# Kernel tuning notes

Hardware: AMD Instinct MI355X
Metric: run time of the kernel (lower is better)

The kernel has to match this reference:

```python
import jax, jax.numpy as jnp
import numpy as np

BATCH, SEQ = 4, 2048
D_MODEL, D_STATE, D_CONV, HEADDIM = 512, 128, 4, 64
D_INNER = 1024          # expand * d_model
NHEADS = 16             # d_inner / headdim
CONV_DIM = D_INNER + 2 * D_STATE   # 1280 (ngroups=1)
D_IN_PROJ = 2 * D_INNER + 2 * D_STATE + NHEADS  # 2320


def setup_inputs() -> dict:
    key = jax.random.key(0)
    ks = jax.random.split(key, 7)
    x = jax.random.normal(ks[0], (BATCH, SEQ, D_MODEL), jnp.float32)
    norm_weight = jnp.ones((D_MODEL,), jnp.float32)
    in_proj_w = jax.random.normal(ks[1], (D_IN_PROJ, D_MODEL), jnp.float32) * 0.02
    conv_w = jax.random.normal(ks[2], (CONV_DIM, 1, D_CONV), jnp.float32) * 0.2
    conv_b = jnp.zeros((CONV_DIM,), jnp.float32)
    dt_bias = jax.random.normal(ks[3], (NHEADS,), jnp.float32) * 0.1
    A_log = jnp.log(jax.random.uniform(ks[4], (NHEADS,), jnp.float32, 1.0, 16.0))
    D_param = jnp.ones((NHEADS,), jnp.float32)
    gated_norm_weight = jnp.ones((D_INNER,), jnp.float32)
    out_proj_w = jax.random.normal(ks[5], (D_MODEL, D_INNER), jnp.float32) * 0.02
    return dict(x=x, norm_weight=norm_weight, in_proj_w=in_proj_w, conv_w=conv_w,
                conv_b=conv_b, dt_bias=dt_bias, A_log=A_log, D_param=D_param,
                gated_norm_weight=gated_norm_weight, out_proj_w=out_proj_w)


def _rmsnorm(x, w, eps):
    return w * (x * jax.lax.rsqrt(jnp.mean(x * x, axis=-1, keepdims=True) + eps))


def _mamba2_forward(x, norm_weight, in_proj_w, conv_w, conv_b, dt_bias,
                    A_log, D_param, gated_norm_weight, out_proj_w):
    b, l, _ = x.shape
    u = _rmsnorm(x, norm_weight, 1e-6)                       # pre-norm (eps=1e-6)
    zxbcdt = u @ in_proj_w.T                                 # (b,l,2320)
    z = zxbcdt[..., :D_INNER]                                # gate
    xBC = zxbcdt[..., D_INNER:D_INNER + CONV_DIM]            # (b,l,1280)
    dt = zxbcdt[..., D_INNER + CONV_DIM:]                    # (b,l,nheads)
    dt = jax.nn.softplus(dt + dt_bias)

    # causal depthwise conv1d over time + SiLU
    conv = jax.lax.conv_general_dilated(
        xBC.transpose(0, 2, 1), conv_w, window_strides=(1,),
        padding=[(D_CONV - 1, 0)], feature_group_count=CONV_DIM,
        dimension_numbers=('NCH', 'OIH', 'NCH'))
    xBC = jax.nn.silu((conv + conv_b[None, :, None]).transpose(0, 2, 1))

    xs = xBC[..., :D_INNER].reshape(b, l, NHEADS, HEADDIM)   # (b,l,h,p)
    Bmat = xBC[..., D_INNER:D_INNER + D_STATE]               # (b,l,n)
    Cmat = xBC[..., D_INNER + D_STATE:]                      # (b,l,n)

    A = -jnp.exp(A_log)                                      # (h,)
    dA = jnp.exp(dt * A)                                     # (b,l,h)
    dtx = dt[..., None] * xs                                 # (b,l,h,p)

    def step(h, inp):
        dA_t, dtx_t, B_t, C_t = inp                          # (b,h),(b,h,p),(b,n),(b,n)
        h = h * dA_t[..., None, None] + dtx_t[..., None] * B_t[:, None, None, :]
        y = jnp.einsum('bhpn,bn->bhp', h, C_t)
        return h, y

    h0 = jnp.zeros((b, NHEADS, HEADDIM, D_STATE), x.dtype)
    _, ys = jax.lax.scan(step, h0, (dA.transpose(1, 0, 2), dtx.transpose(1, 0, 2, 3),
                                    Bmat.transpose(1, 0, 2), Cmat.transpose(1, 0, 2)))
    y = ys.transpose(1, 0, 2, 3) + xs * D_param[None, None, :, None]  # D skip
    y = y.reshape(b, l, D_INNER)

    y = _rmsnorm(y * jax.nn.silu(z), gated_norm_weight, 1e-5)  # RMSNormGated (eps=1e-5)
    return x + y @ out_proj_w.T                                # residual


def reference(x, norm_weight, in_proj_w, conv_w, conv_b, dt_bias,
              A_log, D_param, gated_norm_weight, out_proj_w):
    return _mamba2_forward(x, norm_weight, in_proj_w, conv_w, conv_b, dt_bias,
                           A_log, D_param, gated_norm_weight, out_proj_w)
```

## Files before the change

### kernel.cpp

```cpp
#include <hip/hip_runtime.h>
#include <cstdint>
#include <cstddef>

#define B_ 4
#define L_ 2048
#define DMODEL 512
#define DINNER 1024
#define DSTATE 128
#define NH 16
#define HD 64
#define CONVDIM 1280
#define NPROJ 2320
#define NPAD 2432
#define ML (B_*L_)
#define Q_ 64
#define NCH 32

typedef __bf16 bf16x8 __attribute__((ext_vector_type(8)));
typedef float f32x4 __attribute__((ext_vector_type(4)));

__device__ __forceinline__ float bf2f(ushort u) {
  union { unsigned int i; float f; } v; v.i = ((unsigned int)u) << 16; return v.f;
}
__device__ __forceinline__ ushort f2bf(float f) {
  union { float f; unsigned int i; } v; v.f = f;
  unsigned int u = v.i;
  unsigned int r = (u + 0x7fffu + ((u >> 16) & 1u)) >> 16;
  return (ushort)r;
}
__device__ __forceinline__ float siluf(float x) { return x / (1.f + __expf(-x)); }

__device__ __forceinline__ void gl_lds16(const void* g, void* l) {
  __builtin_amdgcn_global_load_lds(
      (const __attribute__((address_space(1))) unsigned int*)g,
      (__attribute__((address_space(3))) unsigned int*)l,
      16, 0, 0);
}

__global__ __launch_bounds__(256) void k_cvt(const float* __restrict__ wi, const float* __restrict__ wo,
                                             ushort* __restrict__ oi, ushort* __restrict__ oo) {
  int idx = blockIdx.x * 256 + threadIdx.x;
  const int n1 = NPAD * DMODEL;
  if (idx < n1) {
    int n = idx / DMODEL, k = idx % DMODEL;
    oi[idx] = f2bf((n < NPROJ) ? wi[(size_t)n * DMODEL + k] : 0.f);
  } else {
    int j = idx - n1;
    if (j < DMODEL * DINNER) oo[j] = f2bf(wo[j]);
  }
}

__global__ __launch_bounds__(256) void k_rmsnorm(const float* __restrict__ x, const float* __restrict__ w,
                                                 ushort* __restrict__ u) {
  int row = blockIdx.x * 4 + (threadIdx.x >> 6);
  int lane = threadIdx.x & 63;
  const float* xr = x + (size_t)row * DMODEL + lane * 8;
  float4 a = *(const float4*)xr;
  float4 b = *(const float4*)(xr + 4);
  float ss = a.x*a.x + a.y*a.y + a.z*a.z + a.w*a.w + b.x*b.x + b.y*b.y + b.z*b.z + b.w*b.w;
  ss += __shfl_xor(ss, 1);  ss += __shfl_xor(ss, 2);  ss += __shfl_xor(ss, 4);
  ss += __shfl_xor(ss, 8);  ss += __shfl_xor(ss, 16); ss += __shfl_xor(ss, 32);
  float sc = rsqrtf(ss * (1.f / DMODEL) + 1e-6f);
  const float* wr = w + lane * 8;
  float4 wa = *(const float4*)wr;
  float4 wb = *(const float4*)(wr + 4);
  union { ushort s[8]; int4 v; } o;
  o.s[0] = f2bf(a.x * wa.x * sc); o.s[1] = f2bf(a.y * wa.y * sc);
  o.s[2] = f2bf(a.z * wa.z * sc); o.s[3] = f2bf(a.w * wa.w * sc);
  o.s[4] = f2bf(b.x * wb.x * sc); o.s[5] = f2bf(b.y * wb.y * sc);
  o.s[6] = f2bf(b.z * wb.z * sc); o.s[7] = f2bf(b.w * wb.w * sc);
  *(int4*)(u + (size_t)row * DMODEL + lane * 8) = o.v;
}

template <int EPI, int BM, int BN, int MR, int NR>
__global__ __launch_bounds__(256) void gemm_bt(const ushort* __restrict__ A, const ushort* __restrict__ Bm,
                                               void* __restrict__ Cout, const float* __restrict__ resid,
                                               int M, int N, int K, int gx) {
  constexpr int WM = MR * 16, WN = NR * 16;
  constexpr int WAVES_N = BN / WN;
  constexpr int CH_A = BM / 8, CH_B = BN / 8;
  constexpr int PER_A = CH_A / 4, PER_B = CH_B / 4;
  constexpr int SL = PER_A + PER_B;
  __shared__ __align__(16) ushort lA[2][BM * 64];
  __shared__ __align__(16) ushort lB[2][BN * 64];
  const int nwg = gridDim.x;
  const int cpx = nwg >> 3;
  const int bid = blockIdx.x;
  const int swz = (bid & 7) * cpx + (bid >> 3);
  const int n0 = (swz % gx) * BN, m0 = (swz / gx) * BM;
  const int t = threadIdx.x;
  const int wave = t >> 6, lane = t & 63;
  const int wr = wave / WAVES_N, wc = wave % WAVES_N;
  const int r3 = lane >> 3;
  const int ce = (((lane & 7) ^ r3) << 3);
  const int nt = K >> 6;
  f32x4 acc[MR][NR] = {};
  auto stage = [&](int buf, int k0) {
#pragma unroll
    for (int i = 0; i < PER_A; ++i) {
      int chunk = wave * PER_A + i;
      int row = chunk * 8 + r3;
      gl_lds16(A + (size_t)(m0 + row) * K + k0 + ce, (char*)&lA[buf][0] + chunk * 1024);
    }
#pragma unroll
    for (int i = 0; i < PER_B; ++i) {
      int chunk = wave * PER_B + i;
      int row = chunk * 8 + r3;
      gl_lds16(Bm + (size_t)(n0 + row) * K + k0 + ce, (char*)&lB[buf][0] + chunk * 1024);
    }
  };
  stage(0, 0);
  const int rsel = lane & 15;
  const int kswz = (lane & 7) << 3;
  for (int kt = 0; kt < nt; ++kt) {
    const int cur = kt & 1;
    if (kt + 1 < nt) {
      stage(cur ^ 1, (kt + 1) << 6);
      if constexpr (SL == 8) asm volatile("s_waitcnt vmcnt(8)" ::: "memory");
      else if constexpr (SL == 6) asm volatile("s_waitcnt vmcnt(6)" ::: "memory");
      else asm volatile("s_waitcnt vmcnt(0)" ::: "memory");
    } else {
      asm volatile("s_waitcnt vmcnt(0)" ::: "memory");
    }
    __builtin_amdgcn_s_barrier();
#pragma unroll
    for (int kk = 0; kk < 64; kk += 32) {
      const int ksel = kk + ((lane >> 4) << 3);
      const int kcol = ksel ^ kswz;
      bf16x8 af[MR], bfr[NR];
#pragma unroll
      for (int m = 0; m < MR; ++m)
        af[m] = *reinterpret_cast<const bf16x8*>(&lA[cur][(wr * WM + m * 16 + rsel) * 64 + kcol]);
#pragma unroll
      for (int n = 0; n < NR; ++n)
        bfr[n] = *reinterpret_cast<const bf16x8*>(&lB[cur][(wc * WN + n * 16 + rsel) * 64 + kcol]);
#pragma unroll
      for (int m = 0; m < MR; ++m)
#pragma unroll
        for (int n = 0; n < NR; ++n)
          acc[m][n] = __builtin_amdgcn_mfma_f32_16x16x32_bf16(af[m], bfr[n], acc[m][n], 0, 0, 0);
    }
    __builtin_amdgcn_s_barrier();
  }
  const int rowf = (lane >> 4) * 4;
  const int coln = lane & 15;
#pragma unroll
  for (int m = 0; m < MR; ++m) {
#pragma unroll
    for (int n = 0; n < NR; ++n) {
      int gm_base = m0 + wr * WM + m * 16 + rowf;
      int gn = n0 + wc * WN + n * 16 + coln;
#pragma unroll
      for (int r = 0; r < 4; ++r) {
        int gm = gm_base + r;
        float v = acc[m][n][r];
        if (EPI == 0) {
          ((ushort*)Cout)[(size_t)gm * N + gn] = f2bf(v);
        } else {
          ((float*)Cout)[(size_t)gm * N + gn] = v + resid[(size_t)gm * N + gn];
        }
      }
    }
  }
}

__global__ __launch_bounds__(256) void k_dtcum(const ushort* __restrict__ zx, const float* __restrict__ dt_bias,
                                               const float* __restrict__ A_log, float* __restrict__ dtb,
                                               float* __restrict__ acum) {
  int gid = blockIdx.x * 4 + (threadIdx.x >> 6);
  int lane = threadIdx.x & 63;
  int c = gid & 31, h = (gid >> 5) & 15, b = gid >> 9;
  int row = b * L_ + c * Q_ + lane;
  float raw = bf2f(zx[(size_t)row * NPAD + DINNER + CONVDIM + h]) + dt_bias[h];
  float dtv = raw > 20.f ? raw : log1pf(expf(raw));
  dtb[(size_t)row * NH + h] = dtv;
  float a = dtv * (-__expf(A_log[h]));
#pragma unroll
  for (int d = 1; d < 64; d <<= 1) {
    float o = __shfl_up(a, d);
    if (lane >= d) a += o;
  }
  acum[(size_t)row * NH + h] = a;
}

__global__ __launch_bounds__(256) void k_conv(const ushort* __restrict__ zx, const float* __restrict__ cw,
                                              const float* __restrict__ cb, ushort* __restrict__ out) {
  int t = blockIdx.x * 256 + threadIdx.x;
  int cg = t % 160;
  int rb = t / 160;
  int c0 = cg * 8;
  int l0 = (rb & 255) * 8;
  int b = rb >> 8;
  float w0[8], w1[8], w2[8], w3[8], bias[8];
#pragma unroll
  for (int j = 0; j < 8; ++j) {
    float4 wv = *(const float4*)(cw + (c0 + j) * 4);
    w0[j] = wv.x; w1[j] = wv.y; w2[j] = wv.z; w3[j] = wv.w;
    bias[j] = cb[c0 + j];
  }
  const ushort* base = zx + (size_t)(b * L_ + l0) * NPAD + DINNER + c0;
  ushort* ob = out + (size_t)(b * L_ + l0) * CONVDIM + c0;
  union U8 { int4 v; ushort s[8]; };
  float h0[8], h1[8], h2[8];
  if (l0 >= 3) {
    U8 a, bb, cc;
    a.v  = *(const int4*)(base - 3 * NPAD);
    bb.v = *(const int4*)(base - 2 * NPAD);
    cc.v = *(const int4*)(base - 1 * NPAD);
#pragma unroll
    for (int j = 0; j < 8; ++j) { h0[j] = bf2f(a.s[j]); h1[j] = bf2f(bb.s[j]); h2[j] = bf2f(cc.s[j]); }
  } else {
#pragma unroll
    for (int j = 0; j < 8; ++j) { h0[j] = 0.f; h1[j] = 0.f; h2[j] = 0.f; }
  }
#pragma unroll
  for (int i = 0; i < 8; ++i) {
    U8 xv, ov;
    xv.v = *(const int4*)(base + (size_t)i * NPAD);
#pragma unroll
    for (int j = 0; j < 8; ++j) {
      float xc = bf2f(xv.s[j]);
      float v = w0[j] * h0[j] + w1[j] * h1[j] + w2[j] * h2[j] + w3[j] * xc + bias[j];
      ov.s[j] = f2bf(siluf(v));
      h0[j] = h1[j]; h1[j] = h2[j]; h2[j] = xc;
    }
    *(int4*)(ob + (size_t)i * CONVDIM) = ov.v;
  }
}

__global__ __launch_bounds__(256) void k_chunk1(const ushort* __restrict__ xbc, const float* __restrict__ dtb,
                                                const float* __restrict__ acum, ushort* __restrict__ Sbuf,
                                                ushort* __restrict__ yb) {
  __shared__ __align__(16) ushort sC[64 * 136];
  __shared__ __align__(16) ushort sB[64 * 136];
  __shared__ __align__(16) ushort sBTW[128 * 72];
  __shared__ __align__(16) ushort sXT[64 * 72];
  __shared__ float sDt[64], sCum[64];
  const int blk = blockIdx.x;
  const int c = blk & 31, h = (blk >> 5) & 15, b = blk >> 9;
  const int row0 = b * L_ + c * Q_;
  const int tid = threadIdx.x;
  const int wave = tid >> 6, lane = tid & 63;
  if (tid < 64) {
    sDt[tid]  = dtb[(size_t)(row0 + tid) * NH + h];
    sCum[tid] = acum[(size_t)(row0 + tid) * NH + h];
  }
  __syncthreads();
  const float T = sCum[63];
#pragma unroll
  for (int i = 0; i < 4; ++i) {
    int idx = i * 256 + tid;
    int r = idx >> 4, n8 = (idx & 15) * 8;
    const ushort* src = xbc + (size_t)(row0 + r) * CONVDIM + DINNER + n8;
    union { int4 v; ushort s[8]; } bv, cv;
    bv.v = *(const int4*)src;
    cv.v = *(const int4*)(src + DSTATE);
    *(int4*)&sB[r * 136 + n8] = bv.v;
    *(int4*)&sC[r * 136 + n8] = cv.v;
    float w = sDt[r] * __expf(T - sCum[r]);
#pragma unroll
    for (int j = 0; j < 8; ++j)
      sBTW[(n8 + j) * 72 + r] = f2bf(bf2f(bv.s[j]) * w);
  }
#pragma unroll
  for (int i = 0; i < 2; ++i) {
    int idx = i * 256 + tid;
    int r = idx >> 3, p8 = (idx & 7) * 8;
    union { int4 v; ushort s[8]; } xv;
    xv.v = *(const int4*)(xbc + (size_t)(row0 + r) * CONVDIM + h * HD + p8);
#pragma unroll
    for (int j = 0; j < 8; ++j) sXT[(p8 + j) * 72 + r] = xv.s[j];
  }
  __syncthreads();
  const int rsel = lane & 15;
  const int t0 = wave * 16;
  f32x4 g[4] = {};
#pragma unroll
  for (int k0 = 0; k0 < 128; k0 += 32) {
    int ksel = k0 + ((lane >> 4) << 3);
    bf16x8 af = *(const bf16x8*)&sC[(t0 + rsel) * 136 + ksel];
#pragma unroll
    for (int s = 0; s < 4; ++s) {
      bf16x8 bf_ = *(const bf16x8*)&sB[(s * 16 + rsel) * 136 + ksel];
      g[s] = __builtin_amdgcn_mfma_f32_16x16x32_bf16(af, bf_, g[s], 0, 0, 0);
    }
  }
  __syncthreads();
  {
    int trow = t0 + ((lane >> 4) << 2);
#pragma unroll
    for (int s = 0; s < 4; ++s) {
      int sc_ = s * 16 + (lane & 15);
      float dts = sDt[sc_], cums = sCum[sc_];
#pragma unroll
      for (int r = 0; r < 4; ++r) {
        int t2 = trow + r;
        float mv = (sc_ <= t2) ? g[s][r] * dts * __expf(sCum[t2] - cums) : 0.f;
        sC[t2 * 136 + sc_] = f2bf(mv);
      }
    }
  }
  __syncthreads();
  f32x4 yi[4] = {};
#pragma unroll
  for (int k0 = 0; k0 < 64; k0 += 32) {
    int ksel = k0 + ((lane >> 4) << 3);
    bf16x8 af = *(const bf16x8*)&sC[(t0 + rsel) * 136 + ksel];
#pragma unroll
    for (int p = 0; p < 4; ++p) {
      bf16x8 bf_ = *(const bf16x8*)&sXT[(p * 16 + rsel) * 72 + ksel];
      yi[p] = __builtin_amdgcn_mfma_f32_16x16x32_bf16(af, bf_, yi[p], 0, 0, 0);
    }
  }
  {
    int trow = t0 + ((lane >> 4) << 2);
#pragma unroll
    for (int p = 0; p < 4; ++p) {
      int pc = p * 16 + (lane & 15);
#pragma unroll
      for (int r = 0; r < 4; ++r)
        yb[(size_t)(row0 + trow + r) * DINNER + h * HD + pc] = f2bf(yi[p][r]);
    }
  }
  f32x4 sa[8] = {};
#pragma unroll
  for (int k0 = 0; k0 < 64; k0 += 32) {
    int ksel = k0 + ((lane >> 4) << 3);
    bf16x8 af = *(const bf16x8*)&sXT[(t0 + rsel) * 72 + ksel];
#pragma unroll
    for (int n = 0; n < 8; ++n) {
      bf16x8 bf_ = *(const bf16x8*)&sBTW[(n * 16 + rsel) * 72 + ksel];
      sa[n] = __builtin_amdgcn_mfma_f32_16x16x32_bf16(af, bf_, sa[n], 0, 0, 0);
    }
  }
  {
    ushort* Sp = Sbuf + (size_t)((b * NH + h) * NCH + c) * (HD * DSTATE);
    int prow = t0 + ((lane >> 4) << 2);
#pragma unroll
    for (int n = 0; n < 8; ++n) {
      int nc = n * 16 + (lane & 15);
#pragma unroll
      for (int r = 0; r < 4; ++r)
        Sp[(prow + r) * DSTATE + nc] = f2bf(sa[n][r]);
    }
  }
}

__global__ __launch_bounds__(256) void k_scan2(ushort* __restrict__ Sbuf, const float* __restrict__ acum) {
  const int blk = blockIdx.x;
  const int ps = blk & 3, bh = blk >> 2;
  const int b = bh >> 4, h = bh & 15;
  const int off = ps * 2048 + threadIdx.x * 8;
  ushort* base = Sbuf + (size_t)bh * NCH * (HD * DSTATE) + off;
  float alphas[NCH];
#pragma unroll
  for (int c = 0; c < NCH; ++c)
    alphas[c] = __expf(acum[(size_t)(b * L_ + c * Q_ + 63) * NH + h]);
  float hreg[8] = {};
  union { int4 v; ushort s[8]; } sv, nx, hv;
  sv.v = *(const int4*)base;
  for (int c = 0; c < NCH; ++c) {
    nx.v = make_int4(0, 0, 0, 0);
    if (c < NCH - 1) nx.v = *(const int4*)(base + (size_t)(c + 1) * (HD * DSTATE));
#pragma unroll
    for (int i = 0; i < 8; ++i) hv.s[i] = f2bf(hreg[i]);
    *(int4*)(base + (size_t)c * (HD * DSTATE)) = hv.v;
#pragma unroll
    for (int i = 0; i < 8; ++i) hreg[i] = fmaf(alphas[c], hreg[i], bf2f(sv.s[i]));
    sv = nx;
  }
}

__global__ __launch_bounds__(256) void k_chunk2(const ushort* __restrict__ xbc, const ushort* __restrict__ Hin,
                                                const float* __restrict__ acum, const float* __restrict__ Dp,
                                                ushort* __restrict__ yb) {
  __shared__ __align__(16) ushort sC[64 * 136];
  __shared__ __align__(16) ushort sH[64 * 136];
  __shared__ __align__(16) ushort sX[64 * 72];
  __shared__ float sCum[64];
  const int blk = blockIdx.x;
  const int c = blk & 31, h = (blk >> 5) & 15, b = blk >> 9;
  const int row0 = b * L_ + c * Q_;
  const int tid = threadIdx.x, wave = tid >> 6, lane = tid & 63;
  if (tid < 64) sCum[tid] = acum[(size_t)(row0 + tid) * NH + h];
  const ushort* Hp = Hin + (size_t)((b * NH + h) * NCH + c) * (HD * DSTATE);
#pragma unroll
  for (int i = 0; i < 4; ++i) {
    int idx = i * 256 + tid;
    int r = idx >> 4, n8 = (idx & 15) * 8;
    *(int4*)&sC[r * 136 + n8] = *(const int4*)(xbc + (size_t)(row0 + r) * CONVDIM + DINNER + DSTATE + n8);
    *(int4*)&sH[r * 136 + n8] = *(const int4*)(Hp + (size_t)r * DSTATE + n8);
  }
#pragma unroll
  for (int i = 0; i < 2; ++i) {
    int idx = i * 256 + tid;
    int r = idx >> 3, p8 = (idx & 7) * 8;
    *(int4*)&sX[r * 72 + p8] = *(const int4*)(xbc + (size_t)(row0 + r) * CONVDIM + h * HD + p8);
  }
  __syncthreads();
  const int rsel = lane & 15, t0 = wave * 16;
  f32x4 acc[4] = {};
#pragma unroll
  for (int k0 = 0; k0 < 128; k0 += 32) {
    int ksel = k0 + ((lane >> 4) << 3);
    bf16x8 af = *(const bf16x8*)&sC[(t0 + rsel) * 136 + ksel];
#pragma unroll
    for (int p = 0; p < 4; ++p) {
      bf16x8 bf_ = *(const bf16x8*)&sH[(p * 16 + rsel) * 136 + ksel];
      acc[p] = __builtin_amdgcn_mfma_f32_16x16x32_bf16(af, bf_, acc[p], 0, 0, 0);
    }
  }
  const float Dh = Dp[h];
  int trow = t0 + ((lane >> 4) << 2);
#pragma unroll
  for (int p = 0; p < 4; ++p) {
    int pc = p * 16 + (lane & 15);
#pragma unroll
    for (int r = 0; r < 4; ++r) {
      int t2 = trow + r;
      size_t yi_ = (size_t)(row0 + t2) * DINNER + h * HD + pc;
      float v = __expf(sCum[t2]) * acc[p][r] + bf2f(yb[yi_]) + Dh * bf2f(sX[t2 * 72 + pc]);
      yb[yi_] = f2bf(v);
    }
  }
}

__global__ __launch_bounds__(256) void k_gnorm(const ushort* __restrict__ y, const ushort* __restrict__ zx,
                                               const float* __restrict__ gw, ushort* __restrict__ normed) {
  int row = blockIdx.x * 4 + (threadIdx.x >> 6);
  int lane = threadIdx.x & 63;
  int j0 = lane * 16;
  const ushort* yr = y + (size_t)row * DINNER + j0;
  union { int4 v; ushort s[8]; } y0, y1;
  y0.v = *(const int4*)yr;
  y1.v = *(const int4*)(yr + 8);
  const ushort* zr = zx + (size_t)row * NPAD + j0;
  union { int4 v; ushort s[8]; } z0, z1;
  z0.v = *(const int4*)zr;
  z1.v = *(const int4*)(zr + 8);
  float yg[16];
  float ss = 0.f;
#pragma unroll
  for (int i = 0; i < 8; ++i) {
    float g = bf2f(y0.s[i]) * siluf(bf2f(z0.s[i]));
    yg[i] = g; ss += g * g;
  }
#pragma unroll
  for (int i = 0; i < 8; ++i) {
    float g = bf2f(y1.s[i]) * siluf(bf2f(z1.s[i]));
    yg[8 + i] = g; ss += g * g;
  }
  ss += __shfl_xor(ss, 1);  ss += __shfl_xor(ss, 2);  ss += __shfl_xor(ss, 4);
  ss += __shfl_xor(ss, 8);  ss += __shfl_xor(ss, 16); ss += __shfl_xor(ss, 32);
  float sc = rsqrtf(ss * (1.f / DINNER) + 1e-5f);
  float gwv[16];
#pragma unroll
  for (int i = 0; i < 4; ++i) *(float4*)&gwv[i * 4] = *(const float4*)(gw + j0 + i * 4);
  union { int4 v; ushort s[8]; } o0, o1;
#pragma unroll
  for (int i = 0; i < 8; ++i) o0.s[i] = f2bf(yg[i] * sc * gwv[i]);
#pragma unroll
  for (int i = 0; i < 8; ++i) o1.s[i] = f2bf(yg[8 + i] * sc * gwv[8 + i]);
  ushort* op = normed + (size_t)row * DINNER + j0;
  *(int4*)op = o0.v;
  *(int4*)(op + 8) = o1.v;
}

extern "C" void kernel_launch(void* const* d_in, const int* in_sizes, int n_in,
                              void* d_out, int out_size, void* d_ws, size_t ws_size,
                              hipStream_t stream) {
  const float* x         = (const float*)d_in[0];
  const float* norm_w    = (const float*)d_in[1];
  const float* in_proj_w = (const float*)d_in[2];
  const float* conv_w    = (const float*)d_in[3];
  const float* conv_b    = (const float*)d_in[4];
  const float* dt_bias   = (const float*)d_in[5];
  const float* A_log     = (const float*)d_in[6];
  const float* D_param   = (const float*)d_in[7];
  const float* gnw       = (const float*)d_in[8];
  const float* out_proj_w= (const float*)d_in[9];

  char* ws = (char*)d_ws;
  ushort* u      = (ushort*)(ws + 0);
  ushort* Wb     = (ushort*)(ws + 8388608);
  ushort* Woutb  = (ushort*)(ws + 10878976);
  float*  dtb    = (float*)(ws + 11927552);
  float*  acum   = (float*)(ws + 12451840);
  ushort* zx     = (ushort*)(ws + 12976128);
  ushort* convo  = (ushort*)(ws + 52822016);
  ushort* yb     = (ushort*)(ws + 73793536);
  ushort* Sbuf   = (ushort*)(ws + 90570752);
  ushort* normed = convo;

  k_cvt<<<(NPAD * DMODEL + DMODEL * DINNER + 255) / 256, 256, 0, stream>>>(in_proj_w, out_proj_w, Wb, Woutb);
  k_rmsnorm<<<ML / 4, 256, 0, stream>>>(x, norm_w, u);
  gemm_bt<0, 128, 128, 4, 4><<<(NPAD / 128) * (ML / 128), 256, 0, stream>>>(u, Wb, (void*)zx, nullptr, ML, NPAD, DMODEL, NPAD / 128);
  k_dtcum<<<512, 256, 0, stream>>>(zx, dt_bias, A_log, dtb, acum);
  k_conv<<<640, 256, 0, stream>>>(zx, conv_w, conv_b, convo);
  k_chunk1<<<2048, 256, 0, stream>>>(convo, dtb, acum, Sbuf, yb);
  k_scan2<<<256, 256, 0, stream>>>(Sbuf, acum);
  k_chunk2<<<2048, 256, 0, stream>>>(convo, Sbuf, acum, D_param, yb);
  k_gnorm<<<ML / 4, 256, 0, stream>>>(yb, zx, gnw, normed);
  gemm_bt<1, 128, 64, 4, 2><<<(DMODEL / 64) * (ML / 128), 256, 0, stream>>>(normed, Woutb, d_out, x, ML, DMODEL, DINNER, DMODEL / 64);
}
```

Before: 160.8 us.

## Use 32x32 MFMA in GEMMs, move intra-chunk output into state-pass kernel, deepen scan prefetch

The GEMM switches from 16x16x32 to 32x32x16 bf16 MFMA tiles, with MR/NR halved so the same block tiling is kept and fewer LDS fragment loads are needed per MFMA. The SSD chunk work is repartitioned: the first kernel now computes only chunk states, and the second kernel computes the intra-chunk diagonal output plus the inter-chunk output in one pass, sharing the C fragments. This removes the write and read-back of partial y through global memory. The state scan also prefetches four chunks ahead instead of one. The risks are higher register pressure from 16-wide accumulators and an sXT transpose in LDS that may cause bank conflicts.

```diff
diff --git a/kernel.cpp b/kernel.cpp
--- a/kernel.cpp
+++ b/kernel.cpp
@@ -18,6 +18,7 @@
 
 typedef __bf16 bf16x8 __attribute__((ext_vector_type(8)));
 typedef float f32x4 __attribute__((ext_vector_type(4)));
+typedef float f32x16 __attribute__((ext_vector_type(16)));
 
 __device__ __forceinline__ float bf2f(ushort u) {
   union { unsigned int i; float f; } v; v.i = ((unsigned int)u) << 16; return v.f;
@@ -76,7 +77,7 @@
 __global__ __launch_bounds__(256) void gemm_bt(const ushort* __restrict__ A, const ushort* __restrict__ Bm,
                                                void* __restrict__ Cout, const float* __restrict__ resid,
                                                int M, int N, int K, int gx) {
-  constexpr int WM = MR * 16, WN = NR * 16;
+  constexpr int WM = MR * 32, WN = NR * 32;
   constexpr int WAVES_N = BN / WN;
   constexpr int CH_A = BM / 8, CH_B = BN / 8;
   constexpr int PER_A = CH_A / 4, PER_B = CH_B / 4;
@@ -94,7 +95,7 @@
   const int r3 = lane >> 3;
   const int ce = (((lane & 7) ^ r3) << 3);
   const int nt = K >> 6;
-  f32x4 acc[MR][NR] = {};
+  f32x16 acc[MR][NR] = {};
   auto stage = [&](int buf, int k0) {
 #pragma unroll
     for (int i = 0; i < PER_A; ++i) {
@@ -110,7 +111,8 @@
     }
   };
   stage(0, 0);
-  const int rsel = lane & 15;
+  const int rsel = lane & 31;
+  const int khi = (lane >> 5) << 3;
   const int kswz = (lane & 7) << 3;
   for (int kt = 0; kt < nt; ++kt) {
     const int cur = kt & 1;
@@ -124,35 +126,34 @@
     }
     __builtin_amdgcn_s_barrier();
 #pragma unroll
-    for (int kk = 0; kk < 64; kk += 32) {
-      const int ksel = kk + ((lane >> 4) << 3);
-      const int kcol = ksel ^ kswz;
+    for (int kk = 0; kk < 64; kk += 16) {
+      const int kcol = (kk + khi) ^ kswz;
       bf16x8 af[MR], bfr[NR];
 #pragma unroll
       for (int m = 0; m < MR; ++m)
-        af[m] = *reinterpret_cast<const bf16x8*>(&lA[cur][(wr * WM + m * 16 + rsel) * 64 + kcol]);
+        af[m] = *reinterpret_cast<const bf16x8*>(&lA[cur][(wr * WM + m * 32 + rsel) * 64 + kcol]);
 #pragma unroll
       for (int n = 0; n < NR; ++n)
-        bfr[n] = *reinterpret_cast<const bf16x8*>(&lB[cur][(wc * WN + n * 16 + rsel) * 64 + kcol]);
+        bfr[n] = *reinterpret_cast<const bf16x8*>(&lB[cur][(wc * WN + n * 32 + rsel) * 64 + kcol]);
 #pragma unroll
       for (int m = 0; m < MR; ++m)
 #pragma unroll
         for (int n = 0; n < NR; ++n)
-          acc[m][n] = __builtin_amdgcn_mfma_f32_16x16x32_bf16(af[m], bfr[n], acc[m][n], 0, 0, 0);
+          acc[m][n] = __builtin_amdgcn_mfma_f32_32x32x16_bf16(af[m], bfr[n], acc[m][n], 0, 0, 0);
     }
     __builtin_amdgcn_s_barrier();
   }
-  const int rowf = (lane >> 4) * 4;
-  const int coln = lane & 15;
+  const int coln = lane & 31;
+  const int rbase = (lane >> 5) << 2;
 #pragma unroll
   for (int m = 0; m < MR; ++m) {
 #pragma unroll
     for (int n = 0; n < NR; ++n) {
-      int gm_base = m0 + wr * WM + m * 16 + rowf;
-      int gn = n0 + wc * WN + n * 16 + coln;
-#pragma unroll
-      for (int r = 0; r < 4; ++r) {
-        int gm = gm_base + r;
+      int gm0 = m0 + wr * WM + m * 32 + rbase;
+      int gn = n0 + wc * WN + n * 32 + coln;
+#pragma unroll
+      for (int r = 0; r < 16; ++r) {
+        int gm = gm0 + (r & 3) + 8 * (r >> 2);
         float v = acc[m][n][r];
         if (EPI == 0) {
           ((ushort*)Cout)[(size_t)gm * N + gn] = f2bf(v);
@@ -228,11 +229,8 @@
   }
 }
 
-__global__ __launch_bounds__(256) void k_chunk1(const ushort* __restrict__ xbc, const float* __restrict__ dtb,
-                                                const float* __restrict__ acum, ushort* __restrict__ Sbuf,
-                                                ushort* __restrict__ yb) {
-  __shared__ __align__(16) ushort sC[64 * 136];
-  __shared__ __align__(16) ushort sB[64 * 136];
+__global__ __launch_bounds__(256) void k_state(const ushort* __restrict__ xbc, const float* __restrict__ dtb,
+                                               const float* __restrict__ acum, ushort* __restrict__ Sbuf) {
   __shared__ __align__(16) ushort sBTW[128 * 72];
   __shared__ __align__(16) ushort sXT[64 * 72];
   __shared__ float sDt[64], sCum[64];
@@ -251,12 +249,8 @@
   for (int i = 0; i < 4; ++i) {
     int idx = i * 256 + tid;
     int r = idx >> 4, n8 = (idx & 15) * 8;
-    const ushort* src = xbc + (size_t)(row0 + r) * CONVDIM + DINNER + n8;
-    union { int4 v; ushort s[8]; } bv, cv;
-    bv.v = *(const int4*)src;
-    cv.v = *(const int4*)(src + DSTATE);
-    *(int4*)&sB[r * 136 + n8] = bv.v;
-    *(int4*)&sC[r * 136 + n8] = cv.v;
+    union { int4 v; ushort s[8]; } bv;
+    bv.v = *(const int4*)(xbc + (size_t)(row0 + r) * CONVDIM + DINNER + n8);
     float w = sDt[r] * __expf(T - sCum[r]);
 #pragma unroll
     for (int j = 0; j < 8; ++j)
@@ -274,54 +268,6 @@
   __syncthreads();
   const int rsel = lane & 15;
   const int t0 = wave * 16;
-  f32x4 g[4] = {};
-#pragma unroll
-  for (int k0 = 0; k0 < 128; k0 += 32) {
-    int ksel = k0 + ((lane >> 4) << 3);
-    bf16x8 af = *(const bf16x8*)&sC[(t0 + rsel) * 136 + ksel];
-#pragma unroll
-    for (int s = 0; s < 4; ++s) {
-      bf16x8 bf_ = *(const bf16x8*)&sB[(s * 16 + rsel) * 136 + ksel];
-      g[s] = __builtin_amdgcn_mfma_f32_16x16x32_bf16(af, bf_, g[s], 0, 0, 0);
-    }
-  }
-  __syncthreads();
-  {
-    int trow = t0 + ((lane >> 4) << 2);
-#pragma unroll
-    for (int s = 0; s < 4; ++s) {
-      int sc_ = s * 16 + (lane & 15);
-      float dts = sDt[sc_], cums = sCum[sc_];
-#pragma unroll
-      for (int r = 0; r < 4; ++r) {
-        int t2 = trow + r;
-        float mv = (sc_ <= t2) ? g[s][r] * dts * __expf(sCum[t2] - cums) : 0.f;
-        sC[t2 * 136 + sc_] = f2bf(mv);
-      }
-    }
-  }
-  __syncthreads();
-  f32x4 yi[4] = {};
-#pragma unroll
-  for (int k0 = 0; k0 < 64; k0 += 32) {
-    int ksel = k0 + ((lane >> 4) << 3);
-    bf16x8 af = *(const bf16x8*)&sC[(t0 + rsel) * 136 + ksel];
-#pragma unroll
-    for (int p = 0; p < 4; ++p) {
-      bf16x8 bf_ = *(const bf16x8*)&sXT[(p * 16 + rsel) * 72 + ksel];
-      yi[p] = __builtin_amdgcn_mfma_f32_16x16x32_bf16(af, bf_, yi[p], 0, 0, 0);
-    }
-  }
-  {
-    int trow = t0 + ((lane >> 4) << 2);
-#pragma unroll
-    for (int p = 0; p < 4; ++p) {
-      int pc = p * 16 + (lane & 15);
-#pragma unroll
-      for (int r = 0; r < 4; ++r)
-        yb[(size_t)(row0 + trow + r) * DINNER + h * HD + pc] = f2bf(yi[p][r]);
-    }
-  }
   f32x4 sa[8] = {};
 #pragma unroll
   for (int k0 = 0; k0 < 64; k0 += 32) {
@@ -333,16 +279,14 @@
       sa[n] = __builtin_amdgcn_mfma_f32_16x16x32_bf16(af, bf_, sa[n], 0, 0, 0);
     }
   }
-  {
-    ushort* Sp = Sbuf + (size_t)((b * NH + h) * NCH + c) * (HD * DSTATE);
-    int prow = t0 + ((lane >> 4) << 2);
-#pragma unroll
-    for (int n = 0; n < 8; ++n) {
-      int nc = n * 16 + (lane & 15);
-#pragma unroll
-      for (int r = 0; r < 4; ++r)
-        Sp[(prow + r) * DSTATE + nc] = f2bf(sa[n][r]);
-    }
+  ushort* Sp = Sbuf + (size_t)((b * NH + h) * NCH + c) * (HD * DSTATE);
+  int prow = t0 + ((lane >> 4) << 2);
+#pragma unroll
+  for (int n = 0; n < 8; ++n) {
+    int nc = n * 16 + (lane & 15);
+#pragma unroll
+    for (int r = 0; r < 4; ++r)
+      Sp[(prow + r) * DSTATE + nc] = f2bf(sa[n][r]);
   }
 }
 
@@ -356,58 +300,100 @@
 #pragma unroll
   for (int c = 0; c < NCH; ++c)
     alphas[c] = __expf(acum[(size_t)(b * L_ + c * Q_ + 63) * NH + h]);
+  union U8 { int4 v; ushort s[8]; };
+  U8 pf[4];
+#pragma unroll
+  for (int i = 0; i < 4; ++i) pf[i].v = *(const int4*)(base + (size_t)i * (HD * DSTATE));
   float hreg[8] = {};
-  union { int4 v; ushort s[8]; } sv, nx, hv;
-  sv.v = *(const int4*)base;
+  U8 hv;
+#pragma unroll
   for (int c = 0; c < NCH; ++c) {
-    nx.v = make_int4(0, 0, 0, 0);
-    if (c < NCH - 1) nx.v = *(const int4*)(base + (size_t)(c + 1) * (HD * DSTATE));
+    U8 cur = pf[c & 3];
+    if (c + 4 < NCH) pf[c & 3].v = *(const int4*)(base + (size_t)(c + 4) * (HD * DSTATE));
 #pragma unroll
     for (int i = 0; i < 8; ++i) hv.s[i] = f2bf(hreg[i]);
     *(int4*)(base + (size_t)c * (HD * DSTATE)) = hv.v;
 #pragma unroll
-    for (int i = 0; i < 8; ++i) hreg[i] = fmaf(alphas[c], hreg[i], bf2f(sv.s[i]));
-    sv = nx;
-  }
-}
-
-__global__ __launch_bounds__(256) void k_chunk2(const ushort* __restrict__ xbc, const ushort* __restrict__ Hin,
-                                                const float* __restrict__ acum, const float* __restrict__ Dp,
-                                                ushort* __restrict__ yb) {
+    for (int i = 0; i < 8; ++i) hreg[i] = fmaf(alphas[c], hreg[i], bf2f(cur.s[i]));
+  }
+}
+
+__global__ __launch_bounds__(256) void k_y(const ushort* __restrict__ xbc, const ushort* __restrict__ Hin,
+                                           const float* __restrict__ dtb, const float* __restrict__ acum,
+                                           const float* __restrict__ Dp, ushort* __restrict__ yb) {
   __shared__ __align__(16) ushort sC[64 * 136];
+  __shared__ __align__(16) ushort sB[64 * 136];
   __shared__ __align__(16) ushort sH[64 * 136];
-  __shared__ __align__(16) ushort sX[64 * 72];
-  __shared__ float sCum[64];
+  __shared__ __align__(16) ushort sXT[64 * 72];
+  __shared__ float sDt[64], sCum[64];
   const int blk = blockIdx.x;
   const int c = blk & 31, h = (blk >> 5) & 15, b = blk >> 9;
   const int row0 = b * L_ + c * Q_;
-  const int tid = threadIdx.x, wave = tid >> 6, lane = tid & 63;
-  if (tid < 64) sCum[tid] = acum[(size_t)(row0 + tid) * NH + h];
+  const int tid = threadIdx.x;
+  const int wave = tid >> 6, lane = tid & 63;
+  if (tid < 64) {
+    sDt[tid]  = dtb[(size_t)(row0 + tid) * NH + h];
+    sCum[tid] = acum[(size_t)(row0 + tid) * NH + h];
+  }
   const ushort* Hp = Hin + (size_t)((b * NH + h) * NCH + c) * (HD * DSTATE);
 #pragma unroll
   for (int i = 0; i < 4; ++i) {
     int idx = i * 256 + tid;
     int r = idx >> 4, n8 = (idx & 15) * 8;
-    *(int4*)&sC[r * 136 + n8] = *(const int4*)(xbc + (size_t)(row0 + r) * CONVDIM + DINNER + DSTATE + n8);
+    const ushort* src = xbc + (size_t)(row0 + r) * CONVDIM + DINNER + n8;
+    *(int4*)&sB[r * 136 + n8] = *(const int4*)src;
+    *(int4*)&sC[r * 136 + n8] = *(const int4*)(src + DSTATE);
     *(int4*)&sH[r * 136 + n8] = *(const int4*)(Hp + (size_t)r * DSTATE + n8);
   }
 #pragma unroll
   for (int i = 0; i < 2; ++i) {
     int idx = i * 256 + tid;
     int r = idx >> 3, p8 = (idx & 7) * 8;
-    *(int4*)&sX[r * 72 + p8] = *(const int4*)(xbc + (size_t)(row0 + r) * CONVDIM + h * HD + p8);
+    union { int4 v; ushort s[8]; } xv;
+    xv.v = *(const int4*)(xbc + (size_t)(row0 + r) * CONVDIM + h * HD + p8);
+#pragma unroll
+    for (int j = 0; j < 8; ++j) sXT[(p8 + j) * 72 + r] = xv.s[j];
   }
   __syncthreads();
-  const int rsel = lane & 15, t0 = wave * 16;
-  f32x4 acc[4] = {};
+  const int rsel = lane & 15;
+  const int t0 = wave * 16;
+  f32x4 g[4] = {};
+  f32x4 y2[4] = {};
 #pragma unroll
   for (int k0 = 0; k0 < 128; k0 += 32) {
     int ksel = k0 + ((lane >> 4) << 3);
     bf16x8 af = *(const bf16x8*)&sC[(t0 + rsel) * 136 + ksel];
 #pragma unroll
+    for (int s = 0; s < 4; ++s) {
+      bf16x8 bf_ = *(const bf16x8*)&sB[(s * 16 + rsel) * 136 + ksel];
+      g[s] = __builtin_amdgcn_mfma_f32_16x16x32_bf16(af, bf_, g[s], 0, 0, 0);
+      bf16x8 hf = *(const bf16x8*)&sH[(s * 16 + rsel) * 136 + ksel];
+      y2[s] = __builtin_amdgcn_mfma_f32_16x16x32_bf16(af, hf, y2[s], 0, 0, 0);
+    }
+  }
+  {
+    int trow = t0 + ((lane >> 4) << 2);
+#pragma unroll
+    for (int s = 0; s < 4; ++s) {
+      int sc_ = s * 16 + (lane & 15);
+      float dts = sDt[sc_], cums = sCum[sc_];
+#pragma unroll
+      for (int r = 0; r < 4; ++r) {
+        int t2 = trow + r;
+        float mv = (sc_ <= t2) ? g[s][r] * dts * __expf(sCum[t2] - cums) : 0.f;
+        sC[t2 * 136 + sc_] = f2bf(mv);
+      }
+    }
+  }
+  f32x4 yi[4] = {};
+#pragma unroll
+  for (int k0 = 0; k0 < 64; k0 += 32) {
+    int ksel = k0 + ((lane >> 4) << 3);
+    bf16x8 af = *(const bf16x8*)&sC[(t0 + rsel) * 136 + ksel];
+#pragma unroll
     for (int p = 0; p < 4; ++p) {
-      bf16x8 bf_ = *(const bf16x8*)&sH[(p * 16 + rsel) * 136 + ksel];
-      acc[p] = __builtin_amdgcn_mfma_f32_16x16x32_bf16(af, bf_, acc[p], 0, 0, 0);
+      bf16x8 bf_ = *(const bf16x8*)&sXT[(p * 16 + rsel) * 72 + ksel];
+      yi[p] = __builtin_amdgcn_mfma_f32_16x16x32_bf16(af, bf_, yi[p], 0, 0, 0);
     }
   }
   const float Dh = Dp[h];
@@ -418,9 +404,8 @@
 #pragma unroll
     for (int r = 0; r < 4; ++r) {
       int t2 = trow + r;
-      size_t yi_ = (size_t)(row0 + t2) * DINNER + h * HD + pc;
-      float v = __expf(sCum[t2]) * acc[p][r] + bf2f(yb[yi_]) + Dh * bf2f(sX[t2 * 72 + pc]);
-      yb[yi_] = f2bf(v);
+      float v = yi[p][r] + __expf(sCum[t2]) * y2[p][r] + Dh * bf2f(sXT[pc * 72 + t2]);
+      yb[(size_t)(row0 + t2) * DINNER + h * HD + pc] = f2bf(v);
     }
   }
 }
@@ -494,12 +479,12 @@
 
   k_cvt<<<(NPAD * DMODEL + DMODEL * DINNER + 255) / 256, 256, 0, stream>>>(in_proj_w, out_proj_w, Wb, Woutb);
   k_rmsnorm<<<ML / 4, 256, 0, stream>>>(x, norm_w, u);
-  gemm_bt<0, 128, 128, 4, 4><<<(NPAD / 128) * (ML / 128), 256, 0, stream>>>(u, Wb, (void*)zx, nullptr, ML, NPAD, DMODEL, NPAD / 128);
+  gemm_bt<0, 128, 128, 2, 2><<<(NPAD / 128) * (ML / 128), 256, 0, stream>>>(u, Wb, (void*)zx, nullptr, ML, NPAD, DMODEL, NPAD / 128);
   k_dtcum<<<512, 256, 0, stream>>>(zx, dt_bias, A_log, dtb, acum);
   k_conv<<<640, 256, 0, stream>>>(zx, conv_w, conv_b, convo);
-  k_chunk1<<<2048, 256, 0, stream>>>(convo, dtb, acum, Sbuf, yb);
+  k_state<<<2048, 256, 0, stream>>>(convo, dtb, acum, Sbuf);
   k_scan2<<<256, 256, 0, stream>>>(Sbuf, acum);
-  k_chunk2<<<2048, 256, 0, stream>>>(convo, Sbuf, acum, D_param, yb);
+  k_y<<<2048, 256, 0, stream>>>(convo, Sbuf, dtb, acum, D_param, yb);
   k_gnorm<<<ML / 4, 256, 0, stream>>>(yb, zx, gnw, normed);
-  gemm_bt<1, 128, 64, 4, 2><<<(DMODEL / 64) * (ML / 128), 256, 0, stream>>>(normed, Woutb, d_out, x, ML, DMODEL, DINNER, DMODEL / 64);
-}
+  gemm_bt<1, 128, 64, 2, 1><<<(DMODEL / 64) * (ML / 128), 256, 0, stream>>>(normed, Woutb, d_out, x, ML, DMODEL, DINNER, DMODEL / 64);
+}
```

Measured after the change: 151.9 us. 5.5% less time.
